# Kernel optimization log

Measured on AMD Instinct MI355X. Metric: run time of the kernel, lower is better.

The kernel has to match this reference:

```python
import jax, jax.numpy as jnp
import numpy as np

B, L, N = 16, 512, 5
D_WORD, HID = 200, 768
LN_EPS = 1e-12
INIT_STD = 0.02


def setup_inputs() -> dict:
    key = jax.random.key(0)
    ks = jax.random.split(key, 10)
    layer_output = jax.random.normal(ks[0], (B, L, HID), dtype=jnp.float32)
    word_embeddings = jax.random.normal(ks[1], (B, L, N, D_WORD), dtype=jnp.float32)
    word_mask = jax.random.randint(ks[2], (B, L, N), 0, 2, dtype=jnp.int32)
    # linear layers: torch nn.Linear init ~ U(-1/sqrt(fan_in), 1/sqrt(fan_in))
    w1_bound = 1.0 / np.sqrt(D_WORD)
    w2_bound = 1.0 / np.sqrt(HID)
    W1 = jax.random.uniform(ks[3], (D_WORD, HID), jnp.float32, -w1_bound, w1_bound)
    b1 = jax.random.uniform(ks[4], (HID,), jnp.float32, -w1_bound, w1_bound)
    W2 = jax.random.uniform(ks[5], (HID, HID), jnp.float32, -w2_bound, w2_bound)
    b2 = jax.random.uniform(ks[6], (HID,), jnp.float32, -w2_bound, w2_bound)
    attn_W = jax.random.normal(ks[7], (HID, HID), dtype=jnp.float32) * INIT_STD
    gamma = jnp.ones((HID,), dtype=jnp.float32)
    beta = jnp.zeros((HID,), dtype=jnp.float32)
    return {
        "layer_output": layer_output,
        "word_embeddings": word_embeddings,
        "word_mask": word_mask,
        "W1": W1, "b1": b1, "W2": W2, "b2": b2,
        "attn_W": attn_W, "gamma": gamma, "beta": beta,
    }


def reference(layer_output, word_embeddings, word_mask, W1, b1, W2, b2, attn_W, gamma, beta):
    # MLP over word embeddings: [B,L,N,D_word] -> [B,L,N,HID]
    word_outputs = jnp.tanh(word_embeddings @ W1 + b1) @ W2 + b2
    # dropout is identity in eval mode
    # bilinear attention scores: (layer_output @ attn_W) . word_outputs -> [B,L,N]
    scores = jnp.einsum('bld,de,blne->bln', layer_output, attn_W, word_outputs)
    scores = jnp.where(word_mask != 0, jnp.float32(-1e9), scores)
    attn = jax.nn.softmax(scores, axis=-1)  # [B,L,N]
    weighted = jnp.einsum('bln,blnh->blh', attn, word_outputs)
    out = layer_output + weighted
    # LayerNorm over last dim
    mu = jnp.mean(out, axis=-1, keepdims=True)
    var = jnp.mean(jnp.square(out - mu), axis=-1, keepdims=True)
    out = (out - mu) * jax.lax.rsqrt(var + LN_EPS) * gamma + beta
    return out
```

## Files before the change

kernel.cpp:

```cpp
#include <hip/hip_runtime.h>
#include <hip/hip_bf16.h>

#define HID 768
#define DW  200
#define NW  5


template<int TM>
__global__ __launch_bounds__(256)
void mlp1_kernel(const float* __restrict__ WE,
                 const float* __restrict__ W1,
                 const float* __restrict__ b1,
                 float* __restrict__ TH)
{
    __shared__ __align__(16) float weT[DW][TM];
    const int tid = threadIdx.x;
    const long row0 = (long)blockIdx.x * TM;

    {
        const float4* src = reinterpret_cast<const float4*>(WE + row0 * DW);
        for (int i = tid; i < TM * (DW / 4); i += 256) {
            int t = i / (DW / 4), k4 = i % (DW / 4);
            float4 v = src[(size_t)t * (DW / 4) + k4];
            weT[k4 * 4 + 0][t] = v.x; weT[k4 * 4 + 1][t] = v.y;
            weT[k4 * 4 + 2][t] = v.z; weT[k4 * 4 + 3][t] = v.w;
        }
    }
    __syncthreads();

    float acc[TM][3];
    #pragma unroll
    for (int t = 0; t < TM; ++t) { acc[t][0] = 0.f; acc[t][1] = 0.f; acc[t][2] = 0.f; }

    #pragma unroll 2
    for (int k = 0; k < DW; ++k) {
        float a[TM];
        #pragma unroll
        for (int q = 0; q < TM / 4; ++q) {
            float4 v = *reinterpret_cast<const float4*>(&weT[k][q * 4]);
            a[q * 4 + 0] = v.x; a[q * 4 + 1] = v.y; a[q * 4 + 2] = v.z; a[q * 4 + 3] = v.w;
        }
        float w0 = W1[(size_t)k * HID + tid];
        float w1 = W1[(size_t)k * HID + 256 + tid];
        float w2 = W1[(size_t)k * HID + 512 + tid];
        #pragma unroll
        for (int t = 0; t < TM; ++t) {
            acc[t][0] = fmaf(a[t], w0, acc[t][0]);
            acc[t][1] = fmaf(a[t], w1, acc[t][1]);
            acc[t][2] = fmaf(a[t], w2, acc[t][2]);
        }
    }

    #pragma unroll
    for (int c = 0; c < 3; ++c) {
        int j = c * 256 + tid;
        float bb = b1[j];
        #pragma unroll
        for (int t = 0; t < TM; ++t)
            TH[(row0 + t) * HID + j] = tanhf(acc[t][c] + bb);
    }
}

__global__ __launch_bounds__(256)
void gw_kernel(const float* __restrict__ A,
               const float* __restrict__ W2,
               float* __restrict__ G)
{
    __shared__ __align__(16) float AsT[32][68];
    __shared__ __align__(16) float WsT[32][68];
    const int tid = threadIdx.x;
    const int bd = blockIdx.x / (HID / 64), bh = blockIdx.x % (HID / 64);
    const int d0 = bd * 64, h0 = bh * 64;
    const int tx = tid % 16, ty = tid / 16;

    float acc[4][4];
    #pragma unroll
    for (int i = 0; i < 4; ++i)
        #pragma unroll
        for (int j = 0; j < 4; ++j) acc[i][j] = 0.f;

    for (int e0 = 0; e0 < HID; e0 += 32) {
        __syncthreads();
        #pragma unroll
        for (int q = 0; q < 2; ++q) {
            int idx = q * 256 + tid;
            int r = idx / 8, c4 = idx % 8;
            float4 va = *reinterpret_cast<const float4*>(&A [(size_t)(d0 + r) * HID + e0 + c4 * 4]);
            AsT[c4 * 4 + 0][r] = va.x; AsT[c4 * 4 + 1][r] = va.y;
            AsT[c4 * 4 + 2][r] = va.z; AsT[c4 * 4 + 3][r] = va.w;
            float4 vw = *reinterpret_cast<const float4*>(&W2[(size_t)(h0 + r) * HID + e0 + c4 * 4]);
            WsT[c4 * 4 + 0][r] = vw.x; WsT[c4 * 4 + 1][r] = vw.y;
            WsT[c4 * 4 + 2][r] = vw.z; WsT[c4 * 4 + 3][r] = vw.w;
        }
        __syncthreads();
        #pragma unroll 4
        for (int e = 0; e < 32; ++e) {
            float4 a4 = *reinterpret_cast<const float4*>(&AsT[e][ty * 4]);
            float4 b4 = *reinterpret_cast<const float4*>(&WsT[e][tx * 4]);
            float av[4] = {a4.x, a4.y, a4.z, a4.w};
            float bv[4] = {b4.x, b4.y, b4.z, b4.w};
            #pragma unroll
            for (int i = 0; i < 4; ++i)
                #pragma unroll
                for (int j = 0; j < 4; ++j)
                    acc[i][j] = fmaf(av[i], bv[j], acc[i][j]);
        }
    }
    #pragma unroll
    for (int i = 0; i < 4; ++i) {
        float4 o = {acc[i][0], acc[i][1], acc[i][2], acc[i][3]};
        *reinterpret_cast<float4*>(&G[(size_t)(d0 + ty * 4 + i) * HID + h0 + tx * 4]) = o;
    }
}

template<int TT>
__global__ __launch_bounds__(256)
void proj_kernel(const float* __restrict__ LO,
                 const float* __restrict__ G,
                 float* __restrict__ P2)
{
    __shared__ __align__(16) float loT[HID][TT];
    const int tid = threadIdx.x;
    const long tok0 = (long)blockIdx.x * TT;

    {
        const float4* src = reinterpret_cast<const float4*>(LO + tok0 * HID);
        for (int i = tid; i < TT * (HID / 4); i += 256) {
            int t = i / (HID / 4), k4 = i % (HID / 4);
            float4 v = src[(size_t)t * (HID / 4) + k4];
            loT[k4 * 4 + 0][t] = v.x; loT[k4 * 4 + 1][t] = v.y;
            loT[k4 * 4 + 2][t] = v.z; loT[k4 * 4 + 3][t] = v.w;
        }
    }
    __syncthreads();

    float acc[TT][3];
    #pragma unroll
    for (int t = 0; t < TT; ++t) { acc[t][0] = 0.f; acc[t][1] = 0.f; acc[t][2] = 0.f; }

    #pragma unroll 2
    for (int k = 0; k < HID; ++k) {
        float a[TT];
        #pragma unroll
        for (int q = 0; q < TT / 4; ++q) {
            float4 v = *reinterpret_cast<const float4*>(&loT[k][q * 4]);
            a[q * 4 + 0] = v.x; a[q * 4 + 1] = v.y; a[q * 4 + 2] = v.z; a[q * 4 + 3] = v.w;
        }
        float w0 = G[(size_t)k * HID + tid];
        float w1 = G[(size_t)k * HID + 256 + tid];
        float w2 = G[(size_t)k * HID + 512 + tid];
        #pragma unroll
        for (int t = 0; t < TT; ++t) {
            acc[t][0] = fmaf(a[t], w0, acc[t][0]);
            acc[t][1] = fmaf(a[t], w1, acc[t][1]);
            acc[t][2] = fmaf(a[t], w2, acc[t][2]);
        }
    }

    #pragma unroll
    for (int c = 0; c < 3; ++c)
        #pragma unroll
        for (int t = 0; t < TT; ++t)
            P2[(tok0 + t) * HID + c * 256 + tid] = acc[t][c];
}

template<int TT>
__global__ __launch_bounds__(256)
void attn_ln2_kernel(const float* __restrict__ LO,
                     const float* __restrict__ TH,
                     const float* __restrict__ P2,
                     const int* __restrict__ mask,
                     const float* __restrict__ W2,
                     const float* __restrict__ b2,
                     const float* __restrict__ gamma,
                     const float* __restrict__ beta,
                     float* __restrict__ out)
{
    __shared__ __align__(16) float p2s[TT][HID];
    __shared__ __align__(16) float athT[HID][TT];
    __shared__ float sc_s[TT][NW];
    __shared__ float at_s[TT][NW];
    const int tid = threadIdx.x;
    const long tok0 = (long)blockIdx.x * TT;
    const int wave = tid >> 6, lane = tid & 63;

    {
        const float4* src = reinterpret_cast<const float4*>(P2 + tok0 * HID);
        float4* dst = reinterpret_cast<float4*>(&p2s[0][0]);
        for (int i = tid; i < TT * (HID / 4); i += 256) dst[i] = src[i];
    }
    __syncthreads();

    for (int pr = wave; pr < TT * NW; pr += 4) {
        int t = pr / NW, n = pr % NW;
        const float* th = TH + ((tok0 + t) * NW + n) * (size_t)HID;
        float s = 0.f;
        #pragma unroll
        for (int it = 0; it < HID / 256; ++it) {
            int k0 = lane * 4 + it * 256;
            float4 p4 = *reinterpret_cast<const float4*>(&p2s[t][k0]);
            float4 w4 = *reinterpret_cast<const float4*>(&th[k0]);
            s = fmaf(p4.x, w4.x, s); s = fmaf(p4.y, w4.y, s);
            s = fmaf(p4.z, w4.z, s); s = fmaf(p4.w, w4.w, s);
        }
        #pragma unroll
        for (int off = 32; off; off >>= 1) s += __shfl_xor(s, off);
        if (lane == 0) sc_s[t][n] = s;
    }
    __syncthreads();

    if (tid < TT) {
        float v[NW]; float m = -3.0e38f;
        #pragma unroll
        for (int n = 0; n < NW; ++n) {
            float sv = (mask[(tok0 + tid) * NW + n] != 0) ? -1.0e9f : sc_s[tid][n];
            v[n] = sv; m = fmaxf(m, sv);
        }
        float sum = 0.f;
        #pragma unroll
        for (int n = 0; n < NW; ++n) { float e = expf(v[n] - m); v[n] = e; sum += e; }
        float inv = 1.0f / sum;
        #pragma unroll
        for (int n = 0; n < NW; ++n) at_s[tid][n] = v[n] * inv;
    }
    __syncthreads();

    for (int i = tid; i < TT * HID; i += 256) {
        int t = i / HID, h = i % HID;
        const float* th = TH + ((tok0 + t) * NW) * (size_t)HID + h;
        float v = 0.f;
        #pragma unroll
        for (int n = 0; n < NW; ++n) v = fmaf(at_s[t][n], th[n * HID], v);
        athT[h][t] = v;
    }
    __syncthreads();

    float acc[TT][3];
    #pragma unroll
    for (int t = 0; t < TT; ++t) { acc[t][0] = 0.f; acc[t][1] = 0.f; acc[t][2] = 0.f; }

    #pragma unroll 2
    for (int k = 0; k < HID; ++k) {
        float a[TT];
        #pragma unroll
        for (int q = 0; q < TT / 4; ++q) {
            float4 v = *reinterpret_cast<const float4*>(&athT[k][q * 4]);
            a[q * 4 + 0] = v.x; a[q * 4 + 1] = v.y; a[q * 4 + 2] = v.z; a[q * 4 + 3] = v.w;
        }
        float w0 = W2[(size_t)k * HID + tid];
        float w1 = W2[(size_t)k * HID + 256 + tid];
        float w2 = W2[(size_t)k * HID + 512 + tid];
        #pragma unroll
        for (int t = 0; t < TT; ++t) {
            acc[t][0] = fmaf(a[t], w0, acc[t][0]);
            acc[t][1] = fmaf(a[t], w1, acc[t][1]);
            acc[t][2] = fmaf(a[t], w2, acc[t][2]);
        }
    }
    __syncthreads();

    float* outb = &athT[0][0];
    #pragma unroll
    for (int c = 0; c < 3; ++c) {
        int j = c * 256 + tid;
        float bb = b2[j];
        #pragma unroll
        for (int t = 0; t < TT; ++t)
            outb[t * HID + j] = acc[t][c] + bb + LO[(tok0 + t) * HID + j];
    }
    __syncthreads();

    for (int tt = 0; tt < TT / 4; ++tt) {
        int t = wave * (TT / 4) + tt;
        float vals[HID / 64];
        #pragma unroll
        for (int i = 0; i < HID / 64; ++i) vals[i] = outb[t * HID + lane + i * 64];
        float s = 0.f;
        #pragma unroll
        for (int i = 0; i < HID / 64; ++i) s += vals[i];
        #pragma unroll
        for (int off = 32; off; off >>= 1) s += __shfl_xor(s, off);
        float mu = s * (1.0f / HID);
        float q = 0.f;
        #pragma unroll
        for (int i = 0; i < HID / 64; ++i) { float d = vals[i] - mu; q = fmaf(d, d, q); }
        #pragma unroll
        for (int off = 32; off; off >>= 1) q += __shfl_xor(q, off);
        float rs = rsqrtf(q * (1.0f / HID) + 1e-12f);
        #pragma unroll
        for (int i = 0; i < HID / 64; ++i) {
            int h = lane + i * 64;
            out[(tok0 + t) * HID + h] = (vals[i] - mu) * rs * gamma[h] + beta[h];
        }
    }
}

extern "C" void kernel_launch(void* const* d_in, const int* in_sizes, int n_in,
                              void* d_out, int out_size, void* d_ws, size_t ws_size,
                              hipStream_t stream)
{
    const float* LO    = (const float*)d_in[0];
    const float* WE    = (const float*)d_in[1];
    const int*   mask  = (const int*)  d_in[2];
    const float* W1    = (const float*)d_in[3];
    const float* b1    = (const float*)d_in[4];
    const float* W2    = (const float*)d_in[5];
    const float* b2    = (const float*)d_in[6];
    const float* attnW = (const float*)d_in[7];
    const float* gamma = (const float*)d_in[8];
    const float* beta  = (const float*)d_in[9];
    float* out = (float*)d_out;

    const int R = 16 * 512 * NW;
    const int T = 16 * 512;

    float* TH = (float*)d_ws;
    float* P2 = TH + (size_t)R * HID;
    float* G  = P2 + (size_t)T * HID;

    constexpr int TM = 16;
    constexpr int TT = 8;

    gw_kernel<<<(HID / 64) * (HID / 64), 256, 0, stream>>>(attnW, W2, G);
    mlp1_kernel<TM><<<R / TM, 256, 0, stream>>>(WE, W1, b1, TH);
    proj_kernel<TT><<<T / TT, 256, 0, stream>>>(LO, G, P2);
    attn_ln2_kernel<TT><<<T / TT, 256, 0, stream>>>(LO, TH, P2, mask, W2, b2, gamma, beta, out);
}
```

Before: 808.6 us.

## Fuse first MLP layer into attention kernel, keep tanh activations in registers

Removes the separate mlp1 kernel and its large TH intermediate buffer (B*L*5*768 floats). The fused kernel computes tanh(WE@W1+b1) for 20 word rows per half-block in registers, reduces the scores across waves, applies the softmax, and builds the weighted sum in shared memory before the W2 projection. LayerNorm is changed to a single-pass sum/sum-of-squares reduction. The main cost removed is the write and re-read of the TH buffer. In exchange, register pressure rises (60 accumulators) and occupancy may drop, and single-pass variance is slightly less numerically stable.

Result: faster. 687.7 us (-14.9%).

```diff
diff --git a/kernel.cpp b/kernel.cpp
--- a/kernel.cpp
+++ b/kernel.cpp
@@ -5,61 +5,6 @@
 #define DW  200
 #define NW  5
 
-
-template<int TM>
-__global__ __launch_bounds__(256)
-void mlp1_kernel(const float* __restrict__ WE,
-                 const float* __restrict__ W1,
-                 const float* __restrict__ b1,
-                 float* __restrict__ TH)
-{
-    __shared__ __align__(16) float weT[DW][TM];
-    const int tid = threadIdx.x;
-    const long row0 = (long)blockIdx.x * TM;
-
-    {
-        const float4* src = reinterpret_cast<const float4*>(WE + row0 * DW);
-        for (int i = tid; i < TM * (DW / 4); i += 256) {
-            int t = i / (DW / 4), k4 = i % (DW / 4);
-            float4 v = src[(size_t)t * (DW / 4) + k4];
-            weT[k4 * 4 + 0][t] = v.x; weT[k4 * 4 + 1][t] = v.y;
-            weT[k4 * 4 + 2][t] = v.z; weT[k4 * 4 + 3][t] = v.w;
-        }
-    }
-    __syncthreads();
-
-    float acc[TM][3];
-    #pragma unroll
-    for (int t = 0; t < TM; ++t) { acc[t][0] = 0.f; acc[t][1] = 0.f; acc[t][2] = 0.f; }
-
-    #pragma unroll 2
-    for (int k = 0; k < DW; ++k) {
-        float a[TM];
-        #pragma unroll
-        for (int q = 0; q < TM / 4; ++q) {
-            float4 v = *reinterpret_cast<const float4*>(&weT[k][q * 4]);
-            a[q * 4 + 0] = v.x; a[q * 4 + 1] = v.y; a[q * 4 + 2] = v.z; a[q * 4 + 3] = v.w;
-        }
-        float w0 = W1[(size_t)k * HID + tid];
-        float w1 = W1[(size_t)k * HID + 256 + tid];
-        float w2 = W1[(size_t)k * HID + 512 + tid];
-        #pragma unroll
-        for (int t = 0; t < TM; ++t) {
-            acc[t][0] = fmaf(a[t], w0, acc[t][0]);
-            acc[t][1] = fmaf(a[t], w1, acc[t][1]);
-            acc[t][2] = fmaf(a[t], w2, acc[t][2]);
-        }
-    }
-
-    #pragma unroll
-    for (int c = 0; c < 3; ++c) {
-        int j = c * 256 + tid;
-        float bb = b1[j];
-        #pragma unroll
-        for (int t = 0; t < TM; ++t)
-            TH[(row0 + t) * HID + j] = tanhf(acc[t][c] + bb);
-    }
-}
 
 __global__ __launch_bounds__(256)
 void gw_kernel(const float* __restrict__ A,
@@ -164,133 +109,209 @@
             P2[(tok0 + t) * HID + c * 256 + tid] = acc[t][c];
 }
 
-template<int TT>
 __global__ __launch_bounds__(256)
-void attn_ln2_kernel(const float* __restrict__ LO,
-                     const float* __restrict__ TH,
-                     const float* __restrict__ P2,
-                     const int* __restrict__ mask,
-                     const float* __restrict__ W2,
-                     const float* __restrict__ b2,
-                     const float* __restrict__ gamma,
-                     const float* __restrict__ beta,
-                     float* __restrict__ out)
+void fused_kernel(const float* __restrict__ WE,
+                  const float* __restrict__ W1,
+                  const float* __restrict__ b1,
+                  const float* __restrict__ W2,
+                  const float* __restrict__ b2,
+                  const float* __restrict__ LO,
+                  const float* __restrict__ P2,
+                  const int* __restrict__ mask,
+                  const float* __restrict__ gamma,
+                  const float* __restrict__ beta,
+                  float* __restrict__ out)
 {
-    __shared__ __align__(16) float p2s[TT][HID];
-    __shared__ __align__(16) float athT[HID][TT];
-    __shared__ float sc_s[TT][NW];
-    __shared__ float at_s[TT][NW];
+    __shared__ __align__(16) float weT[DW * 20];
+    __shared__ __align__(16) float p2s[4][HID];
+    __shared__ __align__(16) float athT[HID * 8];
+    __shared__ float red[4][32];
+    __shared__ float sc_s[4][NW];
+    __shared__ float at_s[4][NW];
+    __shared__ float mus[8], rss[8];
+
     const int tid = threadIdx.x;
-    const long tok0 = (long)blockIdx.x * TT;
     const int wave = tid >> 6, lane = tid & 63;
-
-    {
-        const float4* src = reinterpret_cast<const float4*>(P2 + tok0 * HID);
-        float4* dst = reinterpret_cast<float4*>(&p2s[0][0]);
-        for (int i = tid; i < TT * (HID / 4); i += 256) dst[i] = src[i];
+    const long tok0 = (long)blockIdx.x * 8;
+
+    #pragma unroll 1
+    for (int g = 0; g < 2; ++g) {
+        const long tokg = tok0 + g * 4;
+        const long rowg = tokg * NW;
+
+        __syncthreads();
+
+        for (int i = tid; i < 20 * (DW / 4); i += 256) {
+            int r = i / (DW / 4), k4 = i % (DW / 4);
+            float4 v = *reinterpret_cast<const float4*>(&WE[(rowg + r) * DW + k4 * 4]);
+            weT[(k4 * 4 + 0) * 20 + r] = v.x;
+            weT[(k4 * 4 + 1) * 20 + r] = v.y;
+            weT[(k4 * 4 + 2) * 20 + r] = v.z;
+            weT[(k4 * 4 + 3) * 20 + r] = v.w;
+        }
+        {
+            const float4* src = reinterpret_cast<const float4*>(P2 + tokg * HID);
+            float4* dst = reinterpret_cast<float4*>(&p2s[0][0]);
+            for (int i = tid; i < 4 * (HID / 4); i += 256) dst[i] = src[i];
+        }
+        __syncthreads();
+
+        float th[20][3];
+        #pragma unroll
+        for (int r = 0; r < 20; ++r) { th[r][0] = 0.f; th[r][1] = 0.f; th[r][2] = 0.f; }
+
+        #pragma unroll 2
+        for (int k = 0; k < DW; ++k) {
+            float a[20];
+            #pragma unroll
+            for (int q = 0; q < 5; ++q) {
+                float4 v = *reinterpret_cast<const float4*>(&weT[k * 20 + q * 4]);
+                a[q * 4 + 0] = v.x; a[q * 4 + 1] = v.y; a[q * 4 + 2] = v.z; a[q * 4 + 3] = v.w;
+            }
+            float w0 = W1[(size_t)k * HID + tid];
+            float w1 = W1[(size_t)k * HID + 256 + tid];
+            float w2 = W1[(size_t)k * HID + 512 + tid];
+            #pragma unroll
+            for (int r = 0; r < 20; ++r) {
+                th[r][0] = fmaf(a[r], w0, th[r][0]);
+                th[r][1] = fmaf(a[r], w1, th[r][1]);
+                th[r][2] = fmaf(a[r], w2, th[r][2]);
+            }
+        }
+        {
+            float bb0 = b1[tid], bb1 = b1[256 + tid], bb2 = b1[512 + tid];
+            #pragma unroll
+            for (int r = 0; r < 20; ++r) {
+                th[r][0] = tanhf(th[r][0] + bb0);
+                th[r][1] = tanhf(th[r][1] + bb1);
+                th[r][2] = tanhf(th[r][2] + bb2);
+            }
+        }
+
+        {
+            float p2v[4][3];
+            #pragma unroll
+            for (int tt = 0; tt < 4; ++tt) {
+                p2v[tt][0] = p2s[tt][tid];
+                p2v[tt][1] = p2s[tt][256 + tid];
+                p2v[tt][2] = p2s[tt][512 + tid];
+            }
+            #pragma unroll
+            for (int tt = 0; tt < 4; ++tt)
+                #pragma unroll
+                for (int n = 0; n < NW; ++n) {
+                    int r = tt * NW + n;
+                    float s = th[r][0] * p2v[tt][0];
+                    s = fmaf(th[r][1], p2v[tt][1], s);
+                    s = fmaf(th[r][2], p2v[tt][2], s);
+                    #pragma unroll
+                    for (int off = 32; off; off >>= 1) s += __shfl_xor(s, off);
+                    if (lane == 0) red[wave][r] = s;
+                }
+        }
+        __syncthreads();
+        if (tid < 20) {
+            float s = red[0][tid] + red[1][tid] + red[2][tid] + red[3][tid];
+            sc_s[tid / NW][tid % NW] = s;
+        }
+        __syncthreads();
+
+        if (tid < 4) {
+            float v[NW]; float m = -3.0e38f;
+            #pragma unroll
+            for (int n = 0; n < NW; ++n) {
+                float sv = (mask[(tokg + tid) * NW + n] != 0) ? -1.0e9f : sc_s[tid][n];
+                v[n] = sv; m = fmaxf(m, sv);
+            }
+            float sum = 0.f;
+            #pragma unroll
+            for (int n = 0; n < NW; ++n) { float e = expf(v[n] - m); v[n] = e; sum += e; }
+            float inv = 1.0f / sum;
+            #pragma unroll
+            for (int n = 0; n < NW; ++n) at_s[tid][n] = v[n] * inv;
+        }
+        __syncthreads();
+
+        #pragma unroll
+        for (int tt = 0; tt < 4; ++tt) {
+            float a0 = 0.f, a1 = 0.f, a2 = 0.f;
+            #pragma unroll
+            for (int n = 0; n < NW; ++n) {
+                float w = at_s[tt][n];
+                a0 = fmaf(w, th[tt * NW + n][0], a0);
+                a1 = fmaf(w, th[tt * NW + n][1], a1);
+                a2 = fmaf(w, th[tt * NW + n][2], a2);
+            }
+            int col = g * 4 + tt;
+            athT[(0 * 256 + tid) * 8 + col] = a0;
+            athT[(1 * 256 + tid) * 8 + col] = a1;
+            athT[(2 * 256 + tid) * 8 + col] = a2;
+        }
     }
     __syncthreads();
 
-    for (int pr = wave; pr < TT * NW; pr += 4) {
-        int t = pr / NW, n = pr % NW;
-        const float* th = TH + ((tok0 + t) * NW + n) * (size_t)HID;
-        float s = 0.f;
-        #pragma unroll
-        for (int it = 0; it < HID / 256; ++it) {
-            int k0 = lane * 4 + it * 256;
-            float4 p4 = *reinterpret_cast<const float4*>(&p2s[t][k0]);
-            float4 w4 = *reinterpret_cast<const float4*>(&th[k0]);
-            s = fmaf(p4.x, w4.x, s); s = fmaf(p4.y, w4.y, s);
-            s = fmaf(p4.z, w4.z, s); s = fmaf(p4.w, w4.w, s);
-        }
-        #pragma unroll
-        for (int off = 32; off; off >>= 1) s += __shfl_xor(s, off);
-        if (lane == 0) sc_s[t][n] = s;
-    }
-    __syncthreads();
-
-    if (tid < TT) {
-        float v[NW]; float m = -3.0e38f;
-        #pragma unroll
-        for (int n = 0; n < NW; ++n) {
-            float sv = (mask[(tok0 + tid) * NW + n] != 0) ? -1.0e9f : sc_s[tid][n];
-            v[n] = sv; m = fmaxf(m, sv);
-        }
-        float sum = 0.f;
-        #pragma unroll
-        for (int n = 0; n < NW; ++n) { float e = expf(v[n] - m); v[n] = e; sum += e; }
-        float inv = 1.0f / sum;
-        #pragma unroll
-        for (int n = 0; n < NW; ++n) at_s[tid][n] = v[n] * inv;
-    }
-    __syncthreads();
-
-    for (int i = tid; i < TT * HID; i += 256) {
-        int t = i / HID, h = i % HID;
-        const float* th = TH + ((tok0 + t) * NW) * (size_t)HID + h;
-        float v = 0.f;
-        #pragma unroll
-        for (int n = 0; n < NW; ++n) v = fmaf(at_s[t][n], th[n * HID], v);
-        athT[h][t] = v;
-    }
-    __syncthreads();
-
-    float acc[TT][3];
-    #pragma unroll
-    for (int t = 0; t < TT; ++t) { acc[t][0] = 0.f; acc[t][1] = 0.f; acc[t][2] = 0.f; }
-
-    #pragma unroll 2
+    float acc[8][3];
+    #pragma unroll
+    for (int t = 0; t < 8; ++t) { acc[t][0] = 0.f; acc[t][1] = 0.f; acc[t][2] = 0.f; }
+
+    #pragma unroll 4
     for (int k = 0; k < HID; ++k) {
-        float a[TT];
-        #pragma unroll
-        for (int q = 0; q < TT / 4; ++q) {
-            float4 v = *reinterpret_cast<const float4*>(&athT[k][q * 4]);
-            a[q * 4 + 0] = v.x; a[q * 4 + 1] = v.y; a[q * 4 + 2] = v.z; a[q * 4 + 3] = v.w;
-        }
+        float4 a0 = *reinterpret_cast<const float4*>(&athT[k * 8]);
+        float4 a1 = *reinterpret_cast<const float4*>(&athT[k * 8 + 4]);
         float w0 = W2[(size_t)k * HID + tid];
         float w1 = W2[(size_t)k * HID + 256 + tid];
         float w2 = W2[(size_t)k * HID + 512 + tid];
-        #pragma unroll
-        for (int t = 0; t < TT; ++t) {
-            acc[t][0] = fmaf(a[t], w0, acc[t][0]);
-            acc[t][1] = fmaf(a[t], w1, acc[t][1]);
-            acc[t][2] = fmaf(a[t], w2, acc[t][2]);
-        }
+        acc[0][0] = fmaf(a0.x, w0, acc[0][0]); acc[0][1] = fmaf(a0.x, w1, acc[0][1]); acc[0][2] = fmaf(a0.x, w2, acc[0][2]);
+        acc[1][0] = fmaf(a0.y, w0, acc[1][0]); acc[1][1] = fmaf(a0.y, w1, acc[1][1]); acc[1][2] = fmaf(a0.y, w2, acc[1][2]);
+        acc[2][0] = fmaf(a0.z, w0, acc[2][0]); acc[2][1] = fmaf(a0.z, w1, acc[2][1]); acc[2][2] = fmaf(a0.z, w2, acc[2][2]);
+        acc[3][0] = fmaf(a0.w, w0, acc[3][0]); acc[3][1] = fmaf(a0.w, w1, acc[3][1]); acc[3][2] = fmaf(a0.w, w2, acc[3][2]);
+        acc[4][0] = fmaf(a1.x, w0, acc[4][0]); acc[4][1] = fmaf(a1.x, w1, acc[4][1]); acc[4][2] = fmaf(a1.x, w2, acc[4][2]);
+        acc[5][0] = fmaf(a1.y, w0, acc[5][0]); acc[5][1] = fmaf(a1.y, w1, acc[5][1]); acc[5][2] = fmaf(a1.y, w2, acc[5][2]);
+        acc[6][0] = fmaf(a1.z, w0, acc[6][0]); acc[6][1] = fmaf(a1.z, w1, acc[6][1]); acc[6][2] = fmaf(a1.z, w2, acc[6][2]);
+        acc[7][0] = fmaf(a1.w, w0, acc[7][0]); acc[7][1] = fmaf(a1.w, w1, acc[7][1]); acc[7][2] = fmaf(a1.w, w2, acc[7][2]);
+    }
+
+    float v[8][3];
+    {
+        float bb0 = b2[tid], bb1 = b2[256 + tid], bb2 = b2[512 + tid];
+        #pragma unroll
+        for (int t = 0; t < 8; ++t) {
+            v[t][0] = acc[t][0] + bb0 + LO[(tok0 + t) * HID + tid];
+            v[t][1] = acc[t][1] + bb1 + LO[(tok0 + t) * HID + 256 + tid];
+            v[t][2] = acc[t][2] + bb2 + LO[(tok0 + t) * HID + 512 + tid];
+        }
+    }
+
+    #pragma unroll
+    for (int t = 0; t < 8; ++t) {
+        float s = v[t][0] + v[t][1] + v[t][2];
+        float q = v[t][0] * v[t][0];
+        q = fmaf(v[t][1], v[t][1], q);
+        q = fmaf(v[t][2], v[t][2], q);
+        #pragma unroll
+        for (int off = 32; off; off >>= 1) { s += __shfl_xor(s, off); q += __shfl_xor(q, off); }
+        if (lane == 0) { red[wave][t] = s; red[wave][8 + t] = q; }
     }
     __syncthreads();
-
-    float* outb = &athT[0][0];
-    #pragma unroll
-    for (int c = 0; c < 3; ++c) {
-        int j = c * 256 + tid;
-        float bb = b2[j];
-        #pragma unroll
-        for (int t = 0; t < TT; ++t)
-            outb[t * HID + j] = acc[t][c] + bb + LO[(tok0 + t) * HID + j];
+    if (tid < 8) {
+        float S = red[0][tid] + red[1][tid] + red[2][tid] + red[3][tid];
+        float Q = red[0][8 + tid] + red[1][8 + tid] + red[2][8 + tid] + red[3][8 + tid];
+        float mu = S * (1.0f / HID);
+        float var = Q * (1.0f / HID) - mu * mu;
+        mus[tid] = mu;
+        rss[tid] = rsqrtf(var + 1e-12f);
     }
     __syncthreads();
 
-    for (int tt = 0; tt < TT / 4; ++tt) {
-        int t = wave * (TT / 4) + tt;
-        float vals[HID / 64];
-        #pragma unroll
-        for (int i = 0; i < HID / 64; ++i) vals[i] = outb[t * HID + lane + i * 64];
-        float s = 0.f;
-        #pragma unroll
-        for (int i = 0; i < HID / 64; ++i) s += vals[i];
-        #pragma unroll
-        for (int off = 32; off; off >>= 1) s += __shfl_xor(s, off);
-        float mu = s * (1.0f / HID);
-        float q = 0.f;
-        #pragma unroll
-        for (int i = 0; i < HID / 64; ++i) { float d = vals[i] - mu; q = fmaf(d, d, q); }
-        #pragma unroll
-        for (int off = 32; off; off >>= 1) q += __shfl_xor(q, off);
-        float rs = rsqrtf(q * (1.0f / HID) + 1e-12f);
-        #pragma unroll
-        for (int i = 0; i < HID / 64; ++i) {
-            int h = lane + i * 64;
-            out[(tok0 + t) * HID + h] = (vals[i] - mu) * rs * gamma[h] + beta[h];
+    {
+        float g0 = gamma[tid], g1 = gamma[256 + tid], g2 = gamma[512 + tid];
+        float e0 = beta[tid],  e1 = beta[256 + tid],  e2 = beta[512 + tid];
+        #pragma unroll
+        for (int t = 0; t < 8; ++t) {
+            float mu = mus[t], rs = rss[t];
+            out[(tok0 + t) * HID + tid]       = (v[t][0] - mu) * rs * g0 + e0;
+            out[(tok0 + t) * HID + 256 + tid] = (v[t][1] - mu) * rs * g1 + e1;
+            out[(tok0 + t) * HID + 512 + tid] = (v[t][2] - mu) * rs * g2 + e2;
         }
     }
 }
@@ -311,18 +332,12 @@
     const float* beta  = (const float*)d_in[9];
     float* out = (float*)d_out;
 
-    const int R = 16 * 512 * NW;
     const int T = 16 * 512;
 
-    float* TH = (float*)d_ws;
-    float* P2 = TH + (size_t)R * HID;
+    float* P2 = (float*)d_ws;
     float* G  = P2 + (size_t)T * HID;
 
-    constexpr int TM = 16;
-    constexpr int TT = 8;
-
     gw_kernel<<<(HID / 64) * (HID / 64), 256, 0, stream>>>(attnW, W2, G);
-    mlp1_kernel<TM><<<R / TM, 256, 0, stream>>>(WE, W1, b1, TH);
-    proj_kernel<TT><<<T / TT, 256, 0, stream>>>(LO, G, P2);
-    attn_ln2_kernel<TT><<<T / TT, 256, 0, stream>>>(LO, TH, P2, mask, W2, b2, gamma, beta, out);
+    proj_kernel<8><<<T / 8, 256, 0, stream>>>(LO, G, P2);
+    fused_kernel<<<T / 8, 256, 0, stream>>>(WE, W1, b1, W2, b2, LO, P2, mask, gamma, beta, out);
 }
```
